# Kernel optimization log

Hardware: AMD Instinct MI355X
Metric: run time of the kernel (lower is better)

## Reference

```python
import jax, jax.numpy as jnp
import numpy as np

# Config (mirrors init_kwargs)
N_PARTS = 4
N_DATASETS = 4
N_VOLUMES = 12
N_TRANSFORMS = 1
TEMP = 0.1
EPS = 1e-6
BS = N_PARTS * N_DATASETS * N_VOLUMES          # 192
N = BS * (N_TRANSFORMS + 1)                    # 384 total rows
PD = N_PARTS * N_DATASETS                      # 16
C, H, W = 32, 48, 48


def setup_inputs() -> dict:
    key = jax.random.key(0)
    k1, k2 = jax.random.split(key)
    reg_pred = jax.random.normal(k1, (N, C, H, W), dtype=jnp.float32)
    mean_representations = jax.random.normal(k2, (N_DATASETS, C, H, W), dtype=jnp.float32)
    return {"reg_pred": reg_pred, "mean_representations": mean_representations}


def reference(reg_pred, mean_representations):
    X = reg_pred.reshape(N, -1)                                  # [N, D]
    ds_id = (jnp.arange(N) // N_PARTS) % N_DATASETS              # dataset id per row
    Mn = mean_representations.reshape(N_DATASETS, -1)[ds_id]     # [N, D] per-row mean
    Z = X - Mn                                                   # demeaned
    # cosine similarity with per-vector norm clamped at eps (torch CosineSimilarity)
    nrm = jnp.maximum(jnp.linalg.norm(Z, axis=1), EPS)
    Zn = Z / nrm[:, None]
    S = (Zn @ Zn.T) / TEMP                                       # [N, N] scaled cos sims
    E = jnp.exp(S)
    # negative (denominator) set for anchor a: all j with j % PD != a % PD
    rem = jnp.arange(N) % PD
    neg_mask = rem[:, None] != rem[None, :]
    Dsum = jnp.sum(E * neg_mask, axis=1)                         # [N]

    p = jnp.arange(BS)
    i1 = p
    i2 = BS + p
    i3 = (p + PD) % N
    i4 = (BS + p + PD) % N

    def pair_loss(a, b):
        # Faithful to original: BOTH terms use the (a,b) numerator similarity
        num = S[a, b]
        en = jnp.exp(num)
        return -(num - jnp.log(en + Dsum[a])) - (num - jnp.log(en + Dsum[b]))

    total = (pair_loss(i1, i2) + pair_loss(i3, i4)
             + pair_loss(i1, i3) + pair_loss(i2, i4)).sum()
    return total / (N_TRANSFORMS * 3 * BS)
```

## Files before the change

kernel.cpp:

```cpp
#include <hip/hip_runtime.h>
#include <hip/hip_bf16.h>
#include <stdint.h>

#define NR 384
#define DD 73728
#define PDV 16
#define BSV 192
#define KSPLIT 64
#define KCH 1152
#define BK 64

typedef __bf16 bf16;
typedef __attribute__((ext_vector_type(8))) __bf16 bf16x8;
typedef __attribute__((ext_vector_type(4))) float f32x4;

__device__ __forceinline__ void async_copy16(const bf16* g, bf16* l) {
    __builtin_amdgcn_global_load_lds(
        (__attribute__((address_space(1))) void*)g,
        (__attribute__((address_space(3))) void*)l,
        16, 0, 0);
}

__global__ __launch_bounds__(256) void k_demean(const float* __restrict__ X,
                                                const float* __restrict__ M,
                                                bf16* __restrict__ Z) {
    int bx  = blockIdx.x;
    int row = bx / 36;
    int cb  = bx - row * 36;
    int col = (cb << 11) + (threadIdx.x << 3);
    int ds  = (row >> 2) & 3;
    size_t e = (size_t)row * DD + col;
    const float4* xp = (const float4*)(X + e);
    const float4* mp = (const float4*)(M + (size_t)ds * DD + col);
    float4 x0 = xp[0], x1 = xp[1];
    float4 m0 = mp[0], m1 = mp[1];
    bf16x8 z;
    z[0] = (bf16)(x0.x - m0.x);
    z[1] = (bf16)(x0.y - m0.y);
    z[2] = (bf16)(x0.z - m0.z);
    z[3] = (bf16)(x0.w - m0.w);
    z[4] = (bf16)(x1.x - m1.x);
    z[5] = (bf16)(x1.y - m1.y);
    z[6] = (bf16)(x1.z - m1.z);
    z[7] = (bf16)(x1.w - m1.w);
    *(bf16x8*)(Z + e) = z;
}

__global__ __launch_bounds__(256) void k_gram(const bf16* __restrict__ Z,
                                              float* __restrict__ G) {
    __shared__ bf16 ash[128 * BK];
    __shared__ bf16 bsh[128 * BK];
    const int tid  = threadIdx.x;
    const int lane = tid & 63;
    const int w    = tid >> 6;
    const int quad = lane >> 4;
    const int l15  = lane & 15;
    const int wm   = w & 1, wn = w >> 1;

    int bx   = blockIdx.x;
    int tile = bx % 6;
    int ks   = bx / 6;
    int tm = (tile < 3) ? 0 : ((tile < 5) ? 1 : 2);
    int tn = (tile < 3) ? tile : ((tile < 5) ? (tile - 2) : 2);
    int rowA0 = tm * 128, rowB0 = tn * 128;
    size_t k0 = (size_t)ks * KCH;

    f32x4 acc[4][4];
#pragma unroll
    for (int i = 0; i < 4; ++i)
#pragma unroll
        for (int j = 0; j < 4; ++j) acc[i][j] = (f32x4){0.f, 0.f, 0.f, 0.f};

    for (int kb = 0; kb < KCH; kb += BK) {
        size_t kbase = k0 + kb;
        __syncthreads();
#pragma unroll
        for (int t = 0; t < 4; ++t) {
            int S   = t * 256 + tid;
            int row = S >> 3;
            int sp  = S & 7;
            int gs  = sp ^ (row & 7);
            size_t gco = kbase + gs * 8;
            int ldsoff = (t * 256 + w * 64) * 8;
            async_copy16(Z + (size_t)(rowA0 + row) * DD + gco, &ash[ldsoff]);
            async_copy16(Z + (size_t)(rowB0 + row) * DD + gco, &bsh[ldsoff]);
        }
        __syncthreads();

#pragma unroll
        for (int kk = 0; kk < BK; kk += 32) {
            int sgi = (kk >> 5) * 4 + quad;
            bf16x8 af[4], bfv[4];
#pragma unroll
            for (int i = 0; i < 4; ++i) {
                int r = wm * 64 + i * 16 + l15;
                af[i] = *(const bf16x8*)&ash[r * BK + ((sgi ^ (r & 7)) << 3)];
            }
#pragma unroll
            for (int j = 0; j < 4; ++j) {
                int r = wn * 64 + j * 16 + l15;
                bfv[j] = *(const bf16x8*)&bsh[r * BK + ((sgi ^ (r & 7)) << 3)];
            }
#pragma unroll
            for (int i = 0; i < 4; ++i)
#pragma unroll
                for (int j = 0; j < 4; ++j)
                    acc[i][j] = __builtin_amdgcn_mfma_f32_16x16x32_bf16(
                        af[i], bfv[j], acc[i][j], 0, 0, 0);
        }
    }

#pragma unroll
    for (int i = 0; i < 4; ++i) {
        int grow0 = rowA0 + wm * 64 + i * 16 + quad * 4;
#pragma unroll
        for (int j = 0; j < 4; ++j) {
            int gcol = rowB0 + wn * 64 + j * 16 + l15;
#pragma unroll
            for (int r = 0; r < 4; ++r)
                atomicAdd(&G[(size_t)(grow0 + r) * NR + gcol], acc[i][j][r]);
        }
    }
}

__global__ __launch_bounds__(256) void k_symm(float* __restrict__ G,
                                              float* __restrict__ invn) {
    int a = blockIdx.x;
    if (threadIdx.x == 0)
        invn[a] = 1.0f / fmaxf(sqrtf(G[(size_t)a * NR + a]), 1e-6f);
    for (int b = threadIdx.x; b < a; b += 256)
        G[(size_t)a * NR + b] = G[(size_t)b * NR + a];
}

__global__ __launch_bounds__(256) void k_dsum(const float* __restrict__ G,
                                              const float* __restrict__ invn,
                                              float* __restrict__ Ds) {
    const int lane = threadIdx.x & 63;
    const int a    = blockIdx.x * 4 + (threadIdx.x >> 6);
    float ia  = invn[a];
    int arem  = a & 15;
    float acc = 0.0f;
    for (int b = lane; b < NR; b += 64) {
        float s = G[(size_t)a * NR + b] * ia * invn[b] * 10.0f;
        if ((b & 15) != arem) acc += expf(s);
    }
#pragma unroll
    for (int o = 32; o > 0; o >>= 1) acc += __shfl_down(acc, o);
    if (lane == 0) Ds[a] = acc;
}

__device__ __forceinline__ float pairloss(const float* __restrict__ G,
                                          const float* __restrict__ invn,
                                          const float* __restrict__ Ds,
                                          int a, int b) {
    float num = G[(size_t)a * NR + b] * invn[a] * invn[b] * 10.0f;
    float en  = expf(num);
    return -(num - logf(en + Ds[a])) - (num - logf(en + Ds[b]));
}

__global__ __launch_bounds__(256) void k_final(const float* __restrict__ G,
                                               const float* __restrict__ invn,
                                               const float* __restrict__ Ds,
                                               float* __restrict__ out) {
    __shared__ float wred[4];
    const int tid  = threadIdx.x;
    const int lane = tid & 63;
    const int w    = tid >> 6;
    float c = 0.0f;
    if (tid < BSV) {
        int p = tid;
        int i1 = p, i2 = BSV + p;
        int i3 = (p + PDV) % NR, i4 = (BSV + p + PDV) % NR;
        c = pairloss(G, invn, Ds, i1, i2) + pairloss(G, invn, Ds, i3, i4)
          + pairloss(G, invn, Ds, i1, i3) + pairloss(G, invn, Ds, i2, i4);
    }
#pragma unroll
    for (int o = 32; o > 0; o >>= 1) c += __shfl_down(c, o);
    if (lane == 0) wred[w] = c;
    __syncthreads();
    if (tid == 0) {
        float tot = wred[0] + wred[1] + wred[2] + wred[3];
        out[0] = tot / 576.0f;
    }
}

extern "C" void kernel_launch(void* const* d_in, const int* in_sizes, int n_in,
                              void* d_out, int out_size, void* d_ws, size_t ws_size,
                              hipStream_t stream) {
    const float* X = (const float*)d_in[0];
    const float* M = (const float*)d_in[1];
    float* out = (float*)d_out;

    char* ws = (char*)d_ws;
    bf16*  Z    = (bf16*)ws;
    float* G    = (float*)(ws + (size_t)NR * DD * 2);
    float* invn = (float*)(ws + (size_t)NR * DD * 2 + (size_t)NR * NR * 4);
    float* Ds   = invn + NR;

    hipMemsetAsync(G, 0, (size_t)NR * NR * sizeof(float), stream);
    k_demean<<<dim3(NR * 36), dim3(256), 0, stream>>>(X, M, Z);
    k_gram<<<dim3(6 * KSPLIT), dim3(256), 0, stream>>>(Z, G);
    k_symm<<<dim3(NR), dim3(256), 0, stream>>>(G, invn);
    k_dsum<<<dim3(NR / 4), dim3(256), 0, stream>>>(G, invn, Ds);
    k_final<<<dim3(1), dim3(256), 0, stream>>>(G, invn, Ds, out);
}
```

Before: 224.0 us.

## Replace atomic split-K accumulation with partial buffers and a reduction kernel

The split-K factor for the Gram GEMM doubles, so twice as many blocks run, each over half the K range. Each block writes its 128x128 partial tile to a dedicated workspace slice instead of issuing float atomics into G. A new reduction kernel sums the partials, writes both symmetric halves of G and computes the inverse norms, which replaces the memset and the symmetrize kernel. This removes atomic contention and uses more CUs, but adds about 50 MB of partial-buffer writes and reads.

```diff
diff --git a/kernel.cpp b/kernel.cpp
--- a/kernel.cpp
+++ b/kernel.cpp
@@ -6,8 +6,8 @@
 #define DD 73728
 #define PDV 16
 #define BSV 192
-#define KSPLIT 64
-#define KCH 1152
+#define KSPLIT 128
+#define KCH 576
 #define BK 64
 
 typedef __bf16 bf16;
@@ -47,7 +47,7 @@
 }
 
 __global__ __launch_bounds__(256) void k_gram(const bf16* __restrict__ Z,
-                                              float* __restrict__ G) {
+                                              float* __restrict__ Gp) {
     __shared__ bf16 ash[128 * BK];
     __shared__ bf16 bsh[128 * BK];
     const int tid  = threadIdx.x;
@@ -110,26 +110,37 @@
         }
     }
 
+    float* gp = Gp + ((size_t)(ks * 6 + tile) << 14);
 #pragma unroll
     for (int i = 0; i < 4; ++i) {
-        int grow0 = rowA0 + wm * 64 + i * 16 + quad * 4;
+        int lr0 = wm * 64 + i * 16 + quad * 4;
 #pragma unroll
         for (int j = 0; j < 4; ++j) {
-            int gcol = rowB0 + wn * 64 + j * 16 + l15;
+            int lc = wn * 64 + j * 16 + l15;
 #pragma unroll
             for (int r = 0; r < 4; ++r)
-                atomicAdd(&G[(size_t)(grow0 + r) * NR + gcol], acc[i][j][r]);
+                gp[(lr0 + r) * 128 + lc] = acc[i][j][r];
         }
     }
 }
 
-__global__ __launch_bounds__(256) void k_symm(float* __restrict__ G,
-                                              float* __restrict__ invn) {
-    int a = blockIdx.x;
-    if (threadIdx.x == 0)
-        invn[a] = 1.0f / fmaxf(sqrtf(G[(size_t)a * NR + a]), 1e-6f);
-    for (int b = threadIdx.x; b < a; b += 256)
-        G[(size_t)a * NR + b] = G[(size_t)b * NR + a];
+__global__ __launch_bounds__(256) void k_red(const float* __restrict__ Gp,
+                                             float* __restrict__ G,
+                                             float* __restrict__ invn) {
+    int t    = blockIdx.x * 256 + threadIdx.x;
+    int tile = t >> 14;
+    int idx  = t & 16383;
+    int lr   = idx >> 7, lc = idx & 127;
+    const float* p = Gp + ((size_t)tile << 14) + idx;
+    float s = 0.0f;
+#pragma unroll 8
+    for (int ks = 0; ks < KSPLIT; ++ks) s += p[(size_t)ks * 98304];
+    int tm = (tile < 3) ? 0 : ((tile < 5) ? 1 : 2);
+    int tn = (tile < 3) ? tile : ((tile < 5) ? (tile - 2) : 2);
+    int a = tm * 128 + lr, b = tn * 128 + lc;
+    G[(size_t)a * NR + b] = s;
+    G[(size_t)b * NR + a] = s;
+    if (a == b) invn[a] = 1.0f / fmaxf(sqrtf(s), 1e-6f);
 }
 
 __global__ __launch_bounds__(256) void k_dsum(const float* __restrict__ G,
@@ -193,14 +204,14 @@
 
     char* ws = (char*)d_ws;
     bf16*  Z    = (bf16*)ws;
-    float* G    = (float*)(ws + (size_t)NR * DD * 2);
-    float* invn = (float*)(ws + (size_t)NR * DD * 2 + (size_t)NR * NR * 4);
+    float* Gp   = (float*)(ws + (size_t)NR * DD * 2);
+    float* G    = Gp + (size_t)KSPLIT * 6 * 16384;
+    float* invn = G + (size_t)NR * NR;
     float* Ds   = invn + NR;
 
-    hipMemsetAsync(G, 0, (size_t)NR * NR * sizeof(float), stream);
     k_demean<<<dim3(NR * 36), dim3(256), 0, stream>>>(X, M, Z);
-    k_gram<<<dim3(6 * KSPLIT), dim3(256), 0, stream>>>(Z, G);
-    k_symm<<<dim3(NR), dim3(256), 0, stream>>>(G, invn);
+    k_gram<<<dim3(6 * KSPLIT), dim3(256), 0, stream>>>(Z, Gp);
+    k_red<<<dim3(384), dim3(256), 0, stream>>>(Gp, G, invn);
     k_dsum<<<dim3(NR / 4), dim3(256), 0, stream>>>(G, invn, Ds);
     k_final<<<dim3(1), dim3(256), 0, stream>>>(G, invn, Ds, out);
 }
```

Measured after the change: 214.3 us. 4.4% less time.
